# Optimization experiments

Measured on AMD Instinct MI355X. Metric: run time of the kernel, lower is better.

The kernel has to match this reference:

```python
import jax, jax.numpy as jnp
import numpy as np

D_IN = 1024
D_OUT = 1024
SEQ = 4096


def setup_inputs() -> dict:
    key = jax.random.key(0)
    k0, k1, k2, k3 = jax.random.split(key, 4)
    inputs = jax.random.normal(k0, (SEQ, D_IN), dtype=jnp.float32)
    # original uses torch.rand (uniform [0,1)) for weights
    W_q = jax.random.uniform(k1, (D_IN, D_OUT), dtype=jnp.float32)
    W_k = jax.random.uniform(k2, (D_IN, D_OUT), dtype=jnp.float32)
    W_v = jax.random.uniform(k3, (D_IN, D_OUT), dtype=jnp.float32)
    return {"inputs": inputs, "W_q": W_q, "W_k": W_k, "W_v": W_v}


def reference(inputs, W_q, W_k, W_v):
    queries = inputs @ W_q            # [S, d_out]
    keys = inputs @ W_k               # [S, d_out]
    values = inputs @ W_v             # [S, d_out]
    d_k = keys.shape[-1]
    scale = 1.0 / jnp.sqrt(jnp.asarray(d_k, dtype=queries.dtype))
    attn_scores = queries @ keys.T    # [S, S]
    attn_weights = jax.nn.softmax(attn_scores * scale, axis=-1)
    context_vectors = attn_weights @ values  # [S, d_out]
    return context_vectors
```

## Files before the change

### kernel.cpp

```cpp
#include <hip/hip_runtime.h>

typedef unsigned short u16;
typedef __attribute__((ext_vector_type(8))) short bf16x8;
typedef __attribute__((ext_vector_type(16))) float f32x16;

#define SEQ 4096
#define DIM 1024

__device__ __forceinline__ u16 f2bf(float f) {
  unsigned u = __float_as_uint(f);
  return (u16)((u + 0x7fffu + ((u >> 16) & 1u)) >> 16);
}
__device__ __forceinline__ float bf2f(u16 h) {
  return __uint_as_float(((unsigned)h) << 16);
}

__device__ __forceinline__ void gload_lds16(const void* g, void* l) {
  __builtin_amdgcn_global_load_lds(
      (const __attribute__((address_space(1))) void*)g,
      (__attribute__((address_space(3))) void*)l, 16, 0, 0);
}

__device__ __forceinline__ size_t pkoff(int row, int col, int kd) {
  int tile = (row >> 7) * (kd >> 5) + (col >> 5);
  int r7 = row & 127, c5 = col & 31;
  int slot = ((r7 >> 4) << 6) | ((c5 >> 3) << 4) | (r7 & 15);
  return (size_t)tile * 4096 + (size_t)(slot * 8 + (c5 & 7));
}

__device__ __forceinline__ void stage_tile_pk(const u16* __restrict__ g,
                                              u16* lds, int tid) {
  const int w = tid >> 6;
  gload_lds16(g + (size_t)tid * 8, lds + (size_t)(w * 64) * 8);
  gload_lds16(g + (size_t)(256 + tid) * 8, lds + (size_t)(256 + w * 64) * 8);
}

#define MFMA32(a, b, c) __builtin_amdgcn_mfma_f32_32x32x16_bf16((a), (b), (c), 0, 0, 0)

template <int NPAIR>
__device__ __forceinline__ void gemm_multi_pk(
    const u16* A0, const u16* A1, const u16* B0, const u16* B1,
    int nkb, u16* lds, f32x16 (&acc)[2][2]) {
  const int tid = threadIdx.x;
  const int w = tid >> 6, l = tid & 63;
  const int wm = w >> 1, wn = w & 1;
  const int lbase = ((l & 31) >> 4) * 512 + (l >> 5) * 128 + (l & 15) * 8;
  u16* lA0 = lds;
  u16* lB0 = lds + 4096;
  u16* lA1 = lds + 8192;
  u16* lB1 = lds + 12288;

#pragma unroll
  for (int ms = 0; ms < 2; ++ms)
#pragma unroll
    for (int ns = 0; ns < 2; ++ns)
#pragma unroll
      for (int i = 0; i < 16; ++i) acc[ms][ns][i] = 0.f;

  const int ao = wm * 2048 + lbase;
  const int bo = wn * 2048 + lbase;

  for (int kb = 0; kb < nkb; ++kb) {
    stage_tile_pk(A0 + (size_t)kb * 4096, lA0, tid);
    stage_tile_pk(B0 + (size_t)kb * 4096, lB0, tid);
    if constexpr (NPAIR >= 3) {
      stage_tile_pk(A1 + (size_t)kb * 4096, lA1, tid);
      stage_tile_pk(B1 + (size_t)kb * 4096, lB1, tid);
    }
    __syncthreads();
    bf16x8 a0[2][2], b0[2][2];
#pragma unroll
    for (int ms = 0; ms < 2; ++ms)
#pragma unroll
      for (int ks = 0; ks < 2; ++ks) {
        a0[ms][ks] = *(const bf16x8*)(lA0 + ao + ms * 1024 + ks * 256);
        b0[ms][ks] = *(const bf16x8*)(lB0 + bo + ms * 1024 + ks * 256);
      }
#pragma unroll
    for (int ms = 0; ms < 2; ++ms)
#pragma unroll
      for (int ns = 0; ns < 2; ++ns)
#pragma unroll
        for (int ks = 0; ks < 2; ++ks)
          acc[ms][ns] = MFMA32(a0[ms][ks], b0[ns][ks], acc[ms][ns]);
    if constexpr (NPAIR >= 3) {
      bf16x8 b1[2][2];
#pragma unroll
      for (int ns = 0; ns < 2; ++ns)
#pragma unroll
        for (int ks = 0; ks < 2; ++ks)
          b1[ns][ks] = *(const bf16x8*)(lB1 + bo + ns * 1024 + ks * 256);
#pragma unroll
      for (int ms = 0; ms < 2; ++ms)
#pragma unroll
        for (int ns = 0; ns < 2; ++ns)
#pragma unroll
          for (int ks = 0; ks < 2; ++ks)
            acc[ms][ns] = MFMA32(a0[ms][ks], b1[ns][ks], acc[ms][ns]);
      bf16x8 a1[2][2];
#pragma unroll
      for (int ms = 0; ms < 2; ++ms)
#pragma unroll
        for (int ks = 0; ks < 2; ++ks)
          a1[ms][ks] = *(const bf16x8*)(lA1 + ao + ms * 1024 + ks * 256);
#pragma unroll
      for (int ms = 0; ms < 2; ++ms)
#pragma unroll
        for (int ns = 0; ns < 2; ++ns)
#pragma unroll
          for (int ks = 0; ks < 2; ++ks)
            acc[ms][ns] = MFMA32(a1[ms][ks], b0[ns][ks], acc[ms][ns]);
    }
    __syncthreads();
  }
}

__device__ __forceinline__ void gemm_one64(
    const u16* A, const u16* B, int nkb, u16* lds, f32x16 (&acc)[2][2]) {
  const int tid = threadIdx.x;
  const int w = tid >> 6, l = tid & 63;
  const int wm = w >> 1, wn = w & 1;
  const int lbase = ((l & 31) >> 4) * 512 + (l >> 5) * 128 + (l & 15) * 8;
  u16* lA = lds;
  u16* lB = lds + 8192;

#pragma unroll
  for (int ms = 0; ms < 2; ++ms)
#pragma unroll
    for (int ns = 0; ns < 2; ++ns)
#pragma unroll
      for (int i = 0; i < 16; ++i) acc[ms][ns][i] = 0.f;

  const int ao = wm * 2048 + lbase;
  const int bo = wn * 2048 + lbase;

  for (int kb = 0; kb < nkb; kb += 2) {
    stage_tile_pk(A + (size_t)kb * 4096, lA, tid);
    stage_tile_pk(A + (size_t)(kb + 1) * 4096, lA + 4096, tid);
    stage_tile_pk(B + (size_t)kb * 4096, lB, tid);
    stage_tile_pk(B + (size_t)(kb + 1) * 4096, lB + 4096, tid);
    __syncthreads();
#pragma unroll
    for (int ht = 0; ht < 2; ++ht) {
      bf16x8 av[2][2], bv[2][2];
#pragma unroll
      for (int ms = 0; ms < 2; ++ms)
#pragma unroll
        for (int ks = 0; ks < 2; ++ks) {
          av[ms][ks] = *(const bf16x8*)(lA + ht * 4096 + ao + ms * 1024 + ks * 256);
          bv[ms][ks] = *(const bf16x8*)(lB + ht * 4096 + bo + ms * 1024 + ks * 256);
        }
#pragma unroll
      for (int ms = 0; ms < 2; ++ms)
#pragma unroll
        for (int ns = 0; ns < 2; ++ns)
#pragma unroll
          for (int ks = 0; ks < 2; ++ks)
            acc[ms][ns] = MFMA32(av[ms][ks], bv[ns][ks], acc[ms][ns]);
    }
    __syncthreads();
  }
}

#define EPILOGUE_IDX32                                     \
  const int tid = threadIdx.x, w = tid >> 6, l = tid & 63; \
  const int wm = w >> 1, wn = w & 1, r = l & 31, h = l >> 5; (void)tid;


__global__ __launch_bounds__(256) void prep_kernel(
    const float* __restrict__ X,
    const float* __restrict__ W0, const float* __restrict__ W1, const float* __restrict__ W2,
    u16* __restrict__ Xh, u16* __restrict__ Xl,
    u16* __restrict__ H0, u16* __restrict__ L0,
    u16* __restrict__ H1, u16* __restrict__ L1,
    u16* __restrict__ H2) {
  const int z = blockIdx.z;
  const int tx = threadIdx.x, ty = threadIdx.y;
  if (z == 0) {
    int idx = (blockIdx.y * 32 + blockIdx.x) * 256 + ty * 32 + tx;
    int row = idx >> 6;
    int c0 = (idx & 63) * 16;
    bf16x8 h0, h1, l0v, l1v;
#pragma unroll
    for (int j = 0; j < 4; ++j) {
      float4 x = *(const float4*)(X + (size_t)row * DIM + c0 + j * 4);
      u16 hh, ll;
      float v;
      v = x.x; hh = f2bf(v); ll = f2bf(v - bf2f(hh));
      if (j < 2) { h0[j*4+0] = (short)hh; l0v[j*4+0] = (short)ll; } else { h1[(j-2)*4+0] = (short)hh; l1v[(j-2)*4+0] = (short)ll; }
      v = x.y; hh = f2bf(v); ll = f2bf(v - bf2f(hh));
      if (j < 2) { h0[j*4+1] = (short)hh; l0v[j*4+1] = (short)ll; } else { h1[(j-2)*4+1] = (short)hh; l1v[(j-2)*4+1] = (short)ll; }
      v = x.z; hh = f2bf(v); ll = f2bf(v - bf2f(hh));
      if (j < 2) { h0[j*4+2] = (short)hh; l0v[j*4+2] = (short)ll; } else { h1[(j-2)*4+2] = (short)hh; l1v[(j-2)*4+2] = (short)ll; }
      v = x.w; hh = f2bf(v); ll = f2bf(v - bf2f(hh));
      if (j < 2) { h0[j*4+3] = (short)hh; l0v[j*4+3] = (short)ll; } else { h1[(j-2)*4+3] = (short)hh; l1v[(j-2)*4+3] = (short)ll; }
    }
    size_t o0 = pkoff(row, c0, DIM);
    size_t o1 = pkoff(row, c0 + 8, DIM);
    *(bf16x8*)(Xh + o0) = h0;
    *(bf16x8*)(Xl + o0) = l0v;
    *(bf16x8*)(Xh + o1) = h1;
    *(bf16x8*)(Xl + o1) = l1v;
    return;
  }
  __shared__ float t[32][33];
  const float* W = (z == 1) ? W0 : (z == 2) ? W1 : W2;
  u16* H = (z == 1) ? H0 : (z == 2) ? H1 : H2;
  u16* L = (z == 1) ? L0 : (z == 2) ? L1 : nullptr;
  const int i0 = blockIdx.y * 32, o0 = blockIdx.x * 32;
#pragma unroll
  for (int m = 0; m < 4; ++m)
    t[ty + 8 * m][tx] = W[(size_t)(i0 + ty + 8 * m) * DIM + o0 + tx];
  __syncthreads();
#pragma unroll
  for (int m = 0; m < 4; ++m) {
    float v = t[tx][ty + 8 * m];
    u16 h = f2bf(v);
    size_t o = pkoff(o0 + ty + 8 * m, i0 + tx, DIM);
    H[o] = h;
    if (L) L[o] = f2bf(v - bf2f(h));
  }
}

__global__ __launch_bounds__(256) void qkv_kernel(
    const u16* __restrict__ Xh, const u16* __restrict__ Xl,
    const u16* __restrict__ Wh0, const u16* __restrict__ Wl0,
    const u16* __restrict__ Wh1, const u16* __restrict__ Wl1,
    const u16* __restrict__ Wh2,
    u16* __restrict__ Qh, u16* __restrict__ Ql,
    u16* __restrict__ Kh, u16* __restrict__ Kl,
    u16* __restrict__ VT) {
  __shared__ __align__(16) u16 lds[4 * 4096];
  const int z = blockIdx.z;
  f32x16 acc[2][2];
  if (z < 2) {
    const u16* Wh = z ? Wh1 : Wh0;
    const u16* Wl = z ? Wl1 : Wl0;
    const int row0 = blockIdx.y * 128, col0 = blockIdx.x * 128;
    gemm_multi_pk<3>(Xh + (size_t)row0 * DIM, Xl + (size_t)row0 * DIM,
                     Wh + (size_t)col0 * DIM, Wl + (size_t)col0 * DIM,
                     DIM / 32, lds, acc);
    EPILOGUE_IDX32
    u16* H = z ? Kh : Qh;
    u16* L = z ? Kl : Ql;
#pragma unroll
    for (int ms = 0; ms < 2; ++ms)
#pragma unroll
      for (int ns = 0; ns < 2; ++ns)
#pragma unroll
        for (int reg = 0; reg < 16; ++reg) {
          int row = row0 + wm * 64 + ms * 32 + (reg & 3) + 8 * (reg >> 2) + 4 * h;
          int col = col0 + wn * 64 + ns * 32 + r;
          float v = acc[ms][ns][reg];
          u16 hh = f2bf(v);
          size_t o = pkoff(row, col, DIM);
          H[o] = hh;
          L[o] = f2bf(v - bf2f(hh));
        }
  } else {
    const int row0 = blockIdx.x * 128;
    const int col0 = blockIdx.y * 128;
    gemm_one64(Wh2 + (size_t)row0 * DIM, Xh + (size_t)col0 * DIM,
               DIM / 32, lds, acc);
    EPILOGUE_IDX32
#pragma unroll
    for (int ms = 0; ms < 2; ++ms)
#pragma unroll
      for (int ns = 0; ns < 2; ++ns)
#pragma unroll
        for (int reg = 0; reg < 16; ++reg) {
          int row = row0 + wm * 64 + ms * 32 + (reg & 3) + 8 * (reg >> 2) + 4 * h;
          int col = col0 + wn * 64 + ns * 32 + r;
          VT[pkoff(row, col, SEQ)] = f2bf(acc[ms][ns][reg]);
        }
  }
}

__global__ __launch_bounds__(256) void s_kernel(
    const u16* __restrict__ Qh, const u16* __restrict__ Ql,
    const u16* __restrict__ Kh, const u16* __restrict__ Kl,
    float* __restrict__ S) {
  __shared__ __align__(16) u16 lds[4 * 4096];
  const int row0 = blockIdx.y * 128, col0 = blockIdx.x * 128;
  f32x16 acc[2][2];
  gemm_multi_pk<3>(Qh + (size_t)row0 * DIM, Ql + (size_t)row0 * DIM,
                   Kh + (size_t)col0 * DIM, Kl + (size_t)col0 * DIM,
                   DIM / 32, lds, acc);
  EPILOGUE_IDX32
  const float scale = 0.03125f;
#pragma unroll
  for (int ms = 0; ms < 2; ++ms)
#pragma unroll
    for (int ns = 0; ns < 2; ++ns)
#pragma unroll
      for (int reg = 0; reg < 16; ++reg) {
        int row = row0 + wm * 64 + ms * 32 + (reg & 3) + 8 * (reg >> 2) + 4 * h;
        int col = col0 + wn * 64 + ns * 32 + r;
        S[(size_t)row * SEQ + col] = acc[ms][ns][reg] * scale;
      }
}

__global__ __launch_bounds__(256) void softmax_kernel(const float* __restrict__ S,
                                                      u16* __restrict__ P) {
  const int row = blockIdx.x;
  const float* s = S + (size_t)row * SEQ;
  const int tid = threadIdx.x;
  const int c0 = tid * 16;
  float v[16];
  float mx = -3.4e38f;
#pragma unroll
  for (int j = 0; j < 4; ++j) {
    float4 x = *(const float4*)(s + c0 + j * 4);
    v[j * 4 + 0] = x.x; v[j * 4 + 1] = x.y; v[j * 4 + 2] = x.z; v[j * 4 + 3] = x.w;
    mx = fmaxf(mx, fmaxf(fmaxf(x.x, x.y), fmaxf(x.z, x.w)));
  }
#pragma unroll
  for (int off = 32; off; off >>= 1) mx = fmaxf(mx, __shfl_xor(mx, off));
  __shared__ float red[8];
  const int w = tid >> 6, l = tid & 63;
  if (l == 0) red[w] = mx;
  __syncthreads();
  mx = fmaxf(fmaxf(red[0], red[1]), fmaxf(red[2], red[3]));
  float sum = 0.f;
#pragma unroll
  for (int i = 0; i < 16; ++i) {
    v[i] = __expf(v[i] - mx);
    sum += v[i];
  }
#pragma unroll
  for (int off = 32; off; off >>= 1) sum += __shfl_xor(sum, off);
  if (l == 0) red[4 + w] = sum;
  __syncthreads();
  sum = red[4] + red[5] + red[6] + red[7];
  const float inv = 1.f / sum;
  bf16x8 p0, p1;
#pragma unroll
  for (int i = 0; i < 8; ++i) {
    p0[i] = (short)f2bf(v[i] * inv);
    p1[i] = (short)f2bf(v[8 + i] * inv);
  }
  *(bf16x8*)(P + pkoff(row, c0, SEQ)) = p0;
  *(bf16x8*)(P + pkoff(row, c0 + 8, SEQ)) = p1;
}

__global__ __launch_bounds__(256) void o_kernel(const u16* __restrict__ P,
                                                const u16* __restrict__ VT,
                                                float* __restrict__ Opart) {
  __shared__ __align__(16) u16 lds[4 * 4096];
  const int z = blockIdx.z;
  const int row0 = blockIdx.y * 128, col0 = blockIdx.x * 128;
  const u16* A = P + (size_t)row0 * SEQ + (size_t)z * 32 * 4096;
  const u16* B = VT + (size_t)col0 * SEQ + (size_t)z * 32 * 4096;
  f32x16 acc[2][2];
  gemm_one64(A, B, 32, lds, acc);
  EPILOGUE_IDX32
  float* O = Opart + (size_t)z * SEQ * DIM;
#pragma unroll
  for (int ms = 0; ms < 2; ++ms)
#pragma unroll
    for (int ns = 0; ns < 2; ++ns)
#pragma unroll
      for (int reg = 0; reg < 16; ++reg) {
        int row = row0 + wm * 64 + ms * 32 + (reg & 3) + 8 * (reg >> 2) + 4 * h;
        int col = col0 + wn * 64 + ns * 32 + r;
        O[(size_t)row * DIM + col] = acc[ms][ns][reg];
      }
}

__global__ __launch_bounds__(256) void o_reduce_kernel(const float* __restrict__ Op,
                                                       float* __restrict__ O) {
  const size_t N = (size_t)SEQ * DIM;
  size_t i = ((size_t)blockIdx.x * 256 + threadIdx.x) * 4;
  float4 a = *(const float4*)(Op + i);
  float4 b = *(const float4*)(Op + N + i);
  float4 c = *(const float4*)(Op + 2 * N + i);
  float4 d = *(const float4*)(Op + 3 * N + i);
  float4 rr;
  rr.x = (a.x + b.x) + (c.x + d.x);
  rr.y = (a.y + b.y) + (c.y + d.y);
  rr.z = (a.z + b.z) + (c.z + d.z);
  rr.w = (a.w + b.w) + (c.w + d.w);
  *(float4*)(O + i) = rr;
}

extern "C" void kernel_launch(void* const* d_in, const int* in_sizes, int n_in,
                              void* d_out, int out_size, void* d_ws, size_t ws_size,
                              hipStream_t stream) {
  const float* X = (const float*)d_in[0];
  const float* Wq = (const float*)d_in[1];
  const float* Wk = (const float*)d_in[2];
  const float* Wv = (const float*)d_in[3];

  const size_t MB = 1024 * 1024;
  char* w = (char*)d_ws;
  u16* Xh = (u16*)(w + 0 * MB);
  u16* Xl = (u16*)(w + 8 * MB);
  u16* WqhT = (u16*)(w + 16 * MB);
  u16* WqlT = (u16*)(w + 18 * MB);
  u16* WkhT = (u16*)(w + 20 * MB);
  u16* WklT = (u16*)(w + 22 * MB);
  u16* WvhT = (u16*)(w + 24 * MB);
  u16* Qh = (u16*)(w + 26 * MB);
  u16* Ql = (u16*)(w + 34 * MB);
  u16* Kh = (u16*)(w + 42 * MB);
  u16* Kl = (u16*)(w + 50 * MB);
  u16* VT = (u16*)(w + 58 * MB);
  float* S = (float*)(w + 66 * MB);
  u16* P = (u16*)(w + 26 * MB);
  float* Opart = (float*)(w + 66 * MB);

  prep_kernel<<<dim3(32, 32, 4), dim3(32, 8), 0, stream>>>(
      X, Wq, Wk, Wv, Xh, Xl, WqhT, WqlT, WkhT, WklT, WvhT);
  qkv_kernel<<<dim3(DIM / 128, SEQ / 128, 3), 256, 0, stream>>>(
      Xh, Xl, WqhT, WqlT, WkhT, WklT, WvhT, Qh, Ql, Kh, Kl, VT);
  s_kernel<<<dim3(SEQ / 128, SEQ / 128), 256, 0, stream>>>(Qh, Ql, Kh, Kl, S);
  softmax_kernel<<<SEQ, 256, 0, stream>>>(S, P);
  o_kernel<<<dim3(DIM / 128, SEQ / 128, 4), 256, 0, stream>>>(P, VT, Opart);
  o_reduce_kernel<<<(SEQ * DIM) / (256 * 4), 256, 0, stream>>>(Opart, (float*)d_out);
}
```

Baseline: 337.8 us.

## Double-buffer LDS in GEMM loops, split accumulators, halve split-K in O

Restructures the shared GEMM helpers to double-buffer LDS tiles, so the next k-block's global-to-LDS loads are issued before computing on the current buffer, with one barrier per iteration instead of two. MFMAs now go into two independent accumulator sets to break dependency chains, and the sets are summed in the epilogues. The O GEMM split-K drops from 4 to 2, which halves the partial-sum write and reduce traffic but gives fewer blocks. LDS use doubles, occupancy hints of 2 blocks per CU are added, and the extra accumulators raise register pressure.

After: 327.7 us. -3.0%, faster.

```diff
diff --git a/kernel.cpp b/kernel.cpp
--- a/kernel.cpp
+++ b/kernel.cpp
@@ -37,37 +37,45 @@
 
 #define MFMA32(a, b, c) __builtin_amdgcn_mfma_f32_32x32x16_bf16((a), (b), (c), 0, 0, 0)
 
-template <int NPAIR>
-__device__ __forceinline__ void gemm_multi_pk(
+__device__ __forceinline__ void gemm3_db(
     const u16* A0, const u16* A1, const u16* B0, const u16* B1,
-    int nkb, u16* lds, f32x16 (&acc)[2][2]) {
+    int nkb, u16* lds, f32x16 (&accP)[2][2], f32x16 (&accQ)[2][2]) {
   const int tid = threadIdx.x;
   const int w = tid >> 6, l = tid & 63;
   const int wm = w >> 1, wn = w & 1;
   const int lbase = ((l & 31) >> 4) * 512 + (l >> 5) * 128 + (l & 15) * 8;
-  u16* lA0 = lds;
-  u16* lB0 = lds + 4096;
-  u16* lA1 = lds + 8192;
-  u16* lB1 = lds + 12288;
 
 #pragma unroll
   for (int ms = 0; ms < 2; ++ms)
 #pragma unroll
     for (int ns = 0; ns < 2; ++ns)
 #pragma unroll
-      for (int i = 0; i < 16; ++i) acc[ms][ns][i] = 0.f;
+      for (int i = 0; i < 16; ++i) { accP[ms][ns][i] = 0.f; accQ[ms][ns][i] = 0.f; }
 
   const int ao = wm * 2048 + lbase;
   const int bo = wn * 2048 + lbase;
 
+  stage_tile_pk(A0, lds, tid);
+  stage_tile_pk(B0, lds + 4096, tid);
+  stage_tile_pk(A1, lds + 8192, tid);
+  stage_tile_pk(B1, lds + 12288, tid);
+
   for (int kb = 0; kb < nkb; ++kb) {
-    stage_tile_pk(A0 + (size_t)kb * 4096, lA0, tid);
-    stage_tile_pk(B0 + (size_t)kb * 4096, lB0, tid);
-    if constexpr (NPAIR >= 3) {
-      stage_tile_pk(A1 + (size_t)kb * 4096, lA1, tid);
-      stage_tile_pk(B1 + (size_t)kb * 4096, lB1, tid);
+    __syncthreads();
+    if (kb + 1 < nkb) {
+      u16* nb = lds + ((kb + 1) & 1) * 16384;
+      const size_t off = (size_t)(kb + 1) * 4096;
+      stage_tile_pk(A0 + off, nb, tid);
+      stage_tile_pk(B0 + off, nb + 4096, tid);
+      stage_tile_pk(A1 + off, nb + 8192, tid);
+      stage_tile_pk(B1 + off, nb + 12288, tid);
     }
-    __syncthreads();
+    const u16* cb = lds + (kb & 1) * 16384;
+    const u16* lA0 = cb;
+    const u16* lB0 = cb + 4096;
+    const u16* lA1 = cb + 8192;
+    const u16* lB1 = cb + 12288;
+
     bf16x8 a0[2][2], b0[2][2];
 #pragma unroll
     for (int ms = 0; ms < 2; ++ms)
@@ -77,69 +85,77 @@
         b0[ms][ks] = *(const bf16x8*)(lB0 + bo + ms * 1024 + ks * 256);
       }
 #pragma unroll
+    for (int ks = 0; ks < 2; ++ks)
+#pragma unroll
+      for (int ms = 0; ms < 2; ++ms)
+#pragma unroll
+        for (int ns = 0; ns < 2; ++ns)
+          accP[ms][ns] = MFMA32(a0[ms][ks], b0[ns][ks], accP[ms][ns]);
+    bf16x8 b1[2][2];
+#pragma unroll
+    for (int ns = 0; ns < 2; ++ns)
+#pragma unroll
+      for (int ks = 0; ks < 2; ++ks)
+        b1[ns][ks] = *(const bf16x8*)(lB1 + bo + ns * 1024 + ks * 256);
+#pragma unroll
+    for (int ks = 0; ks < 2; ++ks)
+#pragma unroll
+      for (int ms = 0; ms < 2; ++ms)
+#pragma unroll
+        for (int ns = 0; ns < 2; ++ns)
+          accQ[ms][ns] = MFMA32(a0[ms][ks], b1[ns][ks], accQ[ms][ns]);
+    bf16x8 a1[2][2];
+#pragma unroll
     for (int ms = 0; ms < 2; ++ms)
 #pragma unroll
-      for (int ns = 0; ns < 2; ++ns)
-#pragma unroll
-        for (int ks = 0; ks < 2; ++ks)
-          acc[ms][ns] = MFMA32(a0[ms][ks], b0[ns][ks], acc[ms][ns]);
-    if constexpr (NPAIR >= 3) {
-      bf16x8 b1[2][2];
-#pragma unroll
-      for (int ns = 0; ns < 2; ++ns)
-#pragma unroll
-        for (int ks = 0; ks < 2; ++ks)
-          b1[ns][ks] = *(const bf16x8*)(lB1 + bo + ns * 1024 + ks * 256);
+      for (int ks = 0; ks < 2; ++ks)
+        a1[ms][ks] = *(const bf16x8*)(lA1 + ao + ms * 1024 + ks * 256);
+#pragma unroll
+    for (int ks = 0; ks < 2; ++ks)
 #pragma unroll
       for (int ms = 0; ms < 2; ++ms)
 #pragma unroll
         for (int ns = 0; ns < 2; ++ns)
-#pragma unroll
-          for (int ks = 0; ks < 2; ++ks)
-            acc[ms][ns] = MFMA32(a0[ms][ks], b1[ns][ks], acc[ms][ns]);
-      bf16x8 a1[2][2];
-#pragma unroll
-      for (int ms = 0; ms < 2; ++ms)
-#pragma unroll
-        for (int ks = 0; ks < 2; ++ks)
-          a1[ms][ks] = *(const bf16x8*)(lA1 + ao + ms * 1024 + ks * 256);
-#pragma unroll
-      for (int ms = 0; ms < 2; ++ms)
-#pragma unroll
-        for (int ns = 0; ns < 2; ++ns)
-#pragma unroll
-          for (int ks = 0; ks < 2; ++ks)
-            acc[ms][ns] = MFMA32(a1[ms][ks], b0[ns][ks], acc[ms][ns]);
-    }
-    __syncthreads();
-  }
-}
-
-__device__ __forceinline__ void gemm_one64(
-    const u16* A, const u16* B, int nkb, u16* lds, f32x16 (&acc)[2][2]) {
+          accQ[ms][ns] = MFMA32(a1[ms][ks], b0[ns][ks], accQ[ms][ns]);
+  }
+  __syncthreads();
+}
+
+__device__ __forceinline__ void gemm1_db(
+    const u16* A, const u16* B, int nkb, u16* lds,
+    f32x16 (&accP)[2][2], f32x16 (&accQ)[2][2]) {
   const int tid = threadIdx.x;
   const int w = tid >> 6, l = tid & 63;
   const int wm = w >> 1, wn = w & 1;
   const int lbase = ((l & 31) >> 4) * 512 + (l >> 5) * 128 + (l & 15) * 8;
-  u16* lA = lds;
-  u16* lB = lds + 8192;
 
 #pragma unroll
   for (int ms = 0; ms < 2; ++ms)
 #pragma unroll
     for (int ns = 0; ns < 2; ++ns)
 #pragma unroll
-      for (int i = 0; i < 16; ++i) acc[ms][ns][i] = 0.f;
+      for (int i = 0; i < 16; ++i) { accP[ms][ns][i] = 0.f; accQ[ms][ns][i] = 0.f; }
 
   const int ao = wm * 2048 + lbase;
   const int bo = wn * 2048 + lbase;
-
-  for (int kb = 0; kb < nkb; kb += 2) {
-    stage_tile_pk(A + (size_t)kb * 4096, lA, tid);
-    stage_tile_pk(A + (size_t)(kb + 1) * 4096, lA + 4096, tid);
-    stage_tile_pk(B + (size_t)kb * 4096, lB, tid);
-    stage_tile_pk(B + (size_t)(kb + 1) * 4096, lB + 4096, tid);
+  const int nit = nkb >> 1;
+
+  stage_tile_pk(A, lds, tid);
+  stage_tile_pk(A + 4096, lds + 4096, tid);
+  stage_tile_pk(B, lds + 8192, tid);
+  stage_tile_pk(B + 4096, lds + 12288, tid);
+
+  for (int it = 0; it < nit; ++it) {
     __syncthreads();
+    if (it + 1 < nit) {
+      u16* nb = lds + ((it + 1) & 1) * 16384;
+      const size_t off = (size_t)(it + 1) * 8192;
+      stage_tile_pk(A + off, nb, tid);
+      stage_tile_pk(A + off + 4096, nb + 4096, tid);
+      stage_tile_pk(B + off, nb + 8192, tid);
+      stage_tile_pk(B + off + 4096, nb + 12288, tid);
+    }
+    const u16* cb = lds + (it & 1) * 16384;
 #pragma unroll
     for (int ht = 0; ht < 2; ++ht) {
       bf16x8 av[2][2], bv[2][2];
@@ -147,19 +163,20 @@
       for (int ms = 0; ms < 2; ++ms)
 #pragma unroll
         for (int ks = 0; ks < 2; ++ks) {
-          av[ms][ks] = *(const bf16x8*)(lA + ht * 4096 + ao + ms * 1024 + ks * 256);
-          bv[ms][ks] = *(const bf16x8*)(lB + ht * 4096 + bo + ms * 1024 + ks * 256);
+          av[ms][ks] = *(const bf16x8*)(cb + ht * 4096 + ao + ms * 1024 + ks * 256);
+          bv[ms][ks] = *(const bf16x8*)(cb + 8192 + ht * 4096 + bo + ms * 1024 + ks * 256);
         }
-#pragma unroll
-      for (int ms = 0; ms < 2; ++ms)
-#pragma unroll
-        for (int ns = 0; ns < 2; ++ns)
-#pragma unroll
-          for (int ks = 0; ks < 2; ++ks)
+      f32x16 (&acc)[2][2] = ht ? accQ : accP;
+#pragma unroll
+      for (int ks = 0; ks < 2; ++ks)
+#pragma unroll
+        for (int ms = 0; ms < 2; ++ms)
+#pragma unroll
+          for (int ns = 0; ns < 2; ++ns)
             acc[ms][ns] = MFMA32(av[ms][ks], bv[ns][ks], acc[ms][ns]);
     }
-    __syncthreads();
-  }
+  }
+  __syncthreads();
 }
 
 #define EPILOGUE_IDX32                                     \
@@ -180,27 +197,22 @@
     int idx = (blockIdx.y * 32 + blockIdx.x) * 256 + ty * 32 + tx;
     int row = idx >> 6;
     int c0 = (idx & 63) * 16;
-    bf16x8 h0, h1, l0v, l1v;
+    u16 h[16], lo[16];
 #pragma unroll
     for (int j = 0; j < 4; ++j) {
       float4 x = *(const float4*)(X + (size_t)row * DIM + c0 + j * 4);
-      u16 hh, ll;
       float v;
-      v = x.x; hh = f2bf(v); ll = f2bf(v - bf2f(hh));
-      if (j < 2) { h0[j*4+0] = (short)hh; l0v[j*4+0] = (short)ll; } else { h1[(j-2)*4+0] = (short)hh; l1v[(j-2)*4+0] = (short)ll; }
-      v = x.y; hh = f2bf(v); ll = f2bf(v - bf2f(hh));
-      if (j < 2) { h0[j*4+1] = (short)hh; l0v[j*4+1] = (short)ll; } else { h1[(j-2)*4+1] = (short)hh; l1v[(j-2)*4+1] = (short)ll; }
-      v = x.z; hh = f2bf(v); ll = f2bf(v - bf2f(hh));
-      if (j < 2) { h0[j*4+2] = (short)hh; l0v[j*4+2] = (short)ll; } else { h1[(j-2)*4+2] = (short)hh; l1v[(j-2)*4+2] = (short)ll; }
-      v = x.w; hh = f2bf(v); ll = f2bf(v - bf2f(hh));
-      if (j < 2) { h0[j*4+3] = (short)hh; l0v[j*4+3] = (short)ll; } else { h1[(j-2)*4+3] = (short)hh; l1v[(j-2)*4+3] = (short)ll; }
+      v = x.x; h[j*4+0] = f2bf(v); lo[j*4+0] = f2bf(v - bf2f(h[j*4+0]));
+      v = x.y; h[j*4+1] = f2bf(v); lo[j*4+1] = f2bf(v - bf2f(h[j*4+1]));
+      v = x.z; h[j*4+2] = f2bf(v); lo[j*4+2] = f2bf(v - bf2f(h[j*4+2]));
+      v = x.w; h[j*4+3] = f2bf(v); lo[j*4+3] = f2bf(v - bf2f(h[j*4+3]));
     }
     size_t o0 = pkoff(row, c0, DIM);
     size_t o1 = pkoff(row, c0 + 8, DIM);
-    *(bf16x8*)(Xh + o0) = h0;
-    *(bf16x8*)(Xl + o0) = l0v;
-    *(bf16x8*)(Xh + o1) = h1;
-    *(bf16x8*)(Xl + o1) = l1v;
+    *(bf16x8*)(Xh + o0) = *(bf16x8*)(h);
+    *(bf16x8*)(Xl + o0) = *(bf16x8*)(lo);
+    *(bf16x8*)(Xh + o1) = *(bf16x8*)(h + 8);
+    *(bf16x8*)(Xl + o1) = *(bf16x8*)(lo + 8);
     return;
   }
   __shared__ float t[32][33];
@@ -222,7 +234,7 @@
   }
 }
 
-__global__ __launch_bounds__(256) void qkv_kernel(
+__global__ __launch_bounds__(256, 2) void qkv_kernel(
     const u16* __restrict__ Xh, const u16* __restrict__ Xl,
     const u16* __restrict__ Wh0, const u16* __restrict__ Wl0,
     const u16* __restrict__ Wh1, const u16* __restrict__ Wl1,
@@ -230,16 +242,16 @@
     u16* __restrict__ Qh, u16* __restrict__ Ql,
     u16* __restrict__ Kh, u16* __restrict__ Kl,
     u16* __restrict__ VT) {
-  __shared__ __align__(16) u16 lds[4 * 4096];
+  __shared__ __align__(16) u16 lds[2 * 4 * 4096];
   const int z = blockIdx.z;
-  f32x16 acc[2][2];
+  f32x16 accP[2][2], accQ[2][2];
   if (z < 2) {
     const u16* Wh = z ? Wh1 : Wh0;
     const u16* Wl = z ? Wl1 : Wl0;
     const int row0 = blockIdx.y * 128, col0 = blockIdx.x * 128;
-    gemm_multi_pk<3>(Xh + (size_t)row0 * DIM, Xl + (size_t)row0 * DIM,
-                     Wh + (size_t)col0 * DIM, Wl + (size_t)col0 * DIM,
-                     DIM / 32, lds, acc);
+    gemm3_db(Xh + (size_t)row0 * DIM, Xl + (size_t)row0 * DIM,
+             Wh + (size_t)col0 * DIM, Wl + (size_t)col0 * DIM,
+             DIM / 32, lds, accP, accQ);
     EPILOGUE_IDX32
     u16* H = z ? Kh : Qh;
     u16* L = z ? Kl : Ql;
@@ -251,7 +263,7 @@
         for (int reg = 0; reg < 16; ++reg) {
           int row = row0 + wm * 64 + ms * 32 + (reg & 3) + 8 * (reg >> 2) + 4 * h;
           int col = col0 + wn * 64 + ns * 32 + r;
-          float v = acc[ms][ns][reg];
+          float v = accP[ms][ns][reg] + accQ[ms][ns][reg];
           u16 hh = f2bf(v);
           size_t o = pkoff(row, col, DIM);
           H[o] = hh;
@@ -260,8 +272,8 @@
   } else {
     const int row0 = blockIdx.x * 128;
     const int col0 = blockIdx.y * 128;
-    gemm_one64(Wh2 + (size_t)row0 * DIM, Xh + (size_t)col0 * DIM,
-               DIM / 32, lds, acc);
+    gemm1_db(Wh2 + (size_t)row0 * DIM, Xh + (size_t)col0 * DIM,
+             DIM / 32, lds, accP, accQ);
     EPILOGUE_IDX32
 #pragma unroll
     for (int ms = 0; ms < 2; ++ms)
@@ -271,21 +283,21 @@
         for (int reg = 0; reg < 16; ++reg) {
           int row = row0 + wm * 64 + ms * 32 + (reg & 3) + 8 * (reg >> 2) + 4 * h;
           int col = col0 + wn * 64 + ns * 32 + r;
-          VT[pkoff(row, col, SEQ)] = f2bf(acc[ms][ns][reg]);
+          VT[pkoff(row, col, SEQ)] = f2bf(accP[ms][ns][reg] + accQ[ms][ns][reg]);
         }
   }
 }
 
-__global__ __launch_bounds__(256) void s_kernel(
+__global__ __launch_bounds__(256, 2) void s_kernel(
     const u16* __restrict__ Qh, const u16* __restrict__ Ql,
     const u16* __restrict__ Kh, const u16* __restrict__ Kl,
     float* __restrict__ S) {
-  __shared__ __align__(16) u16 lds[4 * 4096];
+  __shared__ __align__(16) u16 lds[2 * 4 * 4096];
   const int row0 = blockIdx.y * 128, col0 = blockIdx.x * 128;
-  f32x16 acc[2][2];
-  gemm_multi_pk<3>(Qh + (size_t)row0 * DIM, Ql + (size_t)row0 * DIM,
-                   Kh + (size_t)col0 * DIM, Kl + (size_t)col0 * DIM,
-                   DIM / 32, lds, acc);
+  f32x16 accP[2][2], accQ[2][2];
+  gemm3_db(Qh + (size_t)row0 * DIM, Ql + (size_t)row0 * DIM,
+           Kh + (size_t)col0 * DIM, Kl + (size_t)col0 * DIM,
+           DIM / 32, lds, accP, accQ);
   EPILOGUE_IDX32
   const float scale = 0.03125f;
 #pragma unroll
@@ -296,7 +308,7 @@
       for (int reg = 0; reg < 16; ++reg) {
         int row = row0 + wm * 64 + ms * 32 + (reg & 3) + 8 * (reg >> 2) + 4 * h;
         int col = col0 + wn * 64 + ns * 32 + r;
-        S[(size_t)row * SEQ + col] = acc[ms][ns][reg] * scale;
+        S[(size_t)row * SEQ + col] = (accP[ms][ns][reg] + accQ[ms][ns][reg]) * scale;
       }
 }
 
@@ -333,26 +345,23 @@
   __syncthreads();
   sum = red[4] + red[5] + red[6] + red[7];
   const float inv = 1.f / sum;
-  bf16x8 p0, p1;
-#pragma unroll
-  for (int i = 0; i < 8; ++i) {
-    p0[i] = (short)f2bf(v[i] * inv);
-    p1[i] = (short)f2bf(v[8 + i] * inv);
-  }
-  *(bf16x8*)(P + pkoff(row, c0, SEQ)) = p0;
-  *(bf16x8*)(P + pkoff(row, c0 + 8, SEQ)) = p1;
-}
-
-__global__ __launch_bounds__(256) void o_kernel(const u16* __restrict__ P,
-                                                const u16* __restrict__ VT,
-                                                float* __restrict__ Opart) {
-  __shared__ __align__(16) u16 lds[4 * 4096];
+  u16 p[16];
+#pragma unroll
+  for (int i = 0; i < 16; ++i) p[i] = f2bf(v[i] * inv);
+  *(bf16x8*)(P + pkoff(row, c0, SEQ)) = *(bf16x8*)(p);
+  *(bf16x8*)(P + pkoff(row, c0 + 8, SEQ)) = *(bf16x8*)(p + 8);
+}
+
+__global__ __launch_bounds__(256, 2) void o_kernel(const u16* __restrict__ P,
+                                                   const u16* __restrict__ VT,
+                                                   float* __restrict__ Opart) {
+  __shared__ __align__(16) u16 lds[2 * 4 * 4096];
   const int z = blockIdx.z;
   const int row0 = blockIdx.y * 128, col0 = blockIdx.x * 128;
-  const u16* A = P + (size_t)row0 * SEQ + (size_t)z * 32 * 4096;
-  const u16* B = VT + (size_t)col0 * SEQ + (size_t)z * 32 * 4096;
-  f32x16 acc[2][2];
-  gemm_one64(A, B, 32, lds, acc);
+  const u16* A = P + (size_t)row0 * SEQ + (size_t)z * 64 * 4096;
+  const u16* B = VT + (size_t)col0 * SEQ + (size_t)z * 64 * 4096;
+  f32x16 accP[2][2], accQ[2][2];
+  gemm1_db(A, B, 64, lds, accP, accQ);
   EPILOGUE_IDX32
   float* O = Opart + (size_t)z * SEQ * DIM;
 #pragma unroll
@@ -363,7 +372,7 @@
       for (int reg = 0; reg < 16; ++reg) {
         int row = row0 + wm * 64 + ms * 32 + (reg & 3) + 8 * (reg >> 2) + 4 * h;
         int col = col0 + wn * 64 + ns * 32 + r;
-        O[(size_t)row * DIM + col] = acc[ms][ns][reg];
+        O[(size_t)row * DIM + col] = accP[ms][ns][reg] + accQ[ms][ns][reg];
       }
 }
 
@@ -373,13 +382,11 @@
   size_t i = ((size_t)blockIdx.x * 256 + threadIdx.x) * 4;
   float4 a = *(const float4*)(Op + i);
   float4 b = *(const float4*)(Op + N + i);
-  float4 c = *(const float4*)(Op + 2 * N + i);
-  float4 d = *(const float4*)(Op + 3 * N + i);
   float4 rr;
-  rr.x = (a.x + b.x) + (c.x + d.x);
-  rr.y = (a.y + b.y) + (c.y + d.y);
-  rr.z = (a.z + b.z) + (c.z + d.z);
-  rr.w = (a.w + b.w) + (c.w + d.w);
+  rr.x = a.x + b.x;
+  rr.y = a.y + b.y;
+  rr.z = a.z + b.z;
+  rr.w = a.w + b.w;
   *(float4*)(O + i) = rr;
 }
 
@@ -415,6 +422,6 @@
       Xh, Xl, WqhT, WqlT, WkhT, WklT, WvhT, Qh, Ql, Kh, Kl, VT);
   s_kernel<<<dim3(SEQ / 128, SEQ / 128), 256, 0, stream>>>(Qh, Ql, Kh, Kl, S);
   softmax_kernel<<<SEQ, 256, 0, stream>>>(S, P);
-  o_kernel<<<dim3(DIM / 128, SEQ / 128, 4), 256, 0, stream>>>(P, VT, Opart);
+  o_kernel<<<dim3(DIM / 128, SEQ / 128, 2), 256, 0, stream>>>(P, VT, Opart);
   o_reduce_kernel<<<(SEQ * DIM) / (256 * 4), 256, 0, stream>>>(Opart, (float*)d_out);
 }
```
